# Optimization experiments

Measured on AMD Instinct MI355X. Metric: run time of the kernel, lower is better.

The kernel has to match this reference:

```python
import jax, jax.numpy as jnp
import numpy as np
import math

B, S, H = 2, 2048, 2048
NH, HD, SLOTS = 16, 128, 16


def setup_inputs() -> dict:
    key = jax.random.key(0)
    k1, k2, k3, k4 = jax.random.split(key, 4)
    return {
        "hidden_states": jax.random.normal(k1, (B, S, H), dtype=jnp.float32),
        "stack": jax.random.normal(k2, (B, S, NH, SLOTS, HD), dtype=jnp.float32),
        "mask": jnp.ones((B, S, NH, SLOTS), dtype=jnp.float32),
        "W_action": jax.random.normal(k3, (3 * NH, H), dtype=jnp.float32) * 0.02,
        "b_action": jnp.zeros((3 * NH,), dtype=jnp.float32),
        "W_gate": jax.random.normal(k4, (1, HD), dtype=jnp.float32) * 0.02,
        "b_gate": jnp.zeros((1,), dtype=jnp.float32),
        "res_weight": jnp.ones((1,), dtype=jnp.float32),
    }


def reference(hidden_states, stack, mask, W_action, b_action, W_gate, b_gate, res_weight):
    b, s, h = hidden_states.shape
    nh, slots, hd = stack.shape[2], stack.shape[3], stack.shape[4]

    # action probabilities: push / pop / no-op per head
    logits = (jnp.einsum('bsh,ah->bsa', hidden_states, W_action) + b_action) / math.sqrt(hd)
    actions = jax.nn.softmax(logits.reshape(b, s, nh, 3), axis=-1)  # [B,S,NH,3]

    k_values = hidden_states.reshape(b, s, nh, hd)

    # shifted stack views (slot axis = 3)
    push_stack = jnp.concatenate([k_values[:, :, :, None, :], stack[:, :, :, :-1, :]], axis=3)
    push_mask = jnp.concatenate([jnp.ones_like(mask[:, :, :, :1]), mask[:, :, :, :-1]], axis=3)
    pop_stack = jnp.concatenate([stack[:, :, :, 1:, :], jnp.zeros_like(stack[:, :, :, :1, :])], axis=3)
    pop_mask = jnp.concatenate([mask[:, :, :, 1:], jnp.zeros_like(mask[:, :, :, :1])], axis=3)

    a_push = actions[:, :, :, 0]
    a_pop = actions[:, :, :, 1]
    a_stay = actions[:, :, :, 2]

    new_stack = (a_push[..., None, None] * push_stack
                 + a_pop[..., None, None] * pop_stack
                 + a_stay[..., None, None] * stack)  # [B,S,NH,SLOTS,HD]
    new_mask = (a_push[..., None] * push_mask
                + a_pop[..., None] * pop_mask
                + a_stay[..., None] * mask)  # [B,S,NH,SLOTS]

    # gated readout over slots
    gate_scores = jnp.einsum('bsnkd,d->bsnk', new_stack, W_gate[0]) + b_gate[0]
    gate_weights = jax.nn.softmax(gate_scores + (1.0 - new_mask) * -1e9, axis=-1)
    memory_output = jnp.einsum('bsnkd,bsnk->bsnd', new_stack, gate_weights).reshape(b, s, h)

    output = memory_output * res_weight + hidden_states
    return output, new_stack, new_mask
```

## Files before the change

kernel.cpp:

```cpp
#include <hip/hip_runtime.h>

#define Bc 2
#define Sc 2048
#define Hc 2048
#define NHc 16
#define HDc 128
#define SLOTSc 16
#define NROWS (Bc * Sc)

typedef float v2f __attribute__((ext_vector_type(2)));

__global__ __launch_bounds__(512, 4) void stack_fused(
    const float* __restrict__ hidden,
    const float* __restrict__ stack,
    const float* __restrict__ mask,
    const float* __restrict__ W_action,
    const float* __restrict__ b_action,
    const float* __restrict__ W_gate,
    const float* __restrict__ b_gate,
    const float* __restrict__ res_weight,
    float* __restrict__ out,
    float* __restrict__ new_stack,
    float* __restrict__ new_mask)
{
    __shared__ float hid[Hc];

    const int bs   = blockIdx.x >> 1;
    const int half = blockIdx.x & 1;
    const int tid  = threadIdx.x;
    const int lane = tid & 63;
    const int wave = tid >> 6;
    const int n    = half * 8 + wave;

    const float4* hrow4 = (const float4*)(hidden + (size_t)bs * Hc);
    ((float4*)hid)[tid] = hrow4[tid];
    __syncthreads();

    float s0 = 0.f, s1 = 0.f, s2 = 0.f;
    {
        const float4* hl = (const float4*)hid;
        const float4* W0 = (const float4*)(W_action + (size_t)(3 * n) * Hc);
        const float4* W1 = W0 + (Hc / 4);
        const float4* W2 = W1 + (Hc / 4);
        #pragma unroll 2
        for (int j = 0; j < 8; ++j) {
            float4 a  = hl[lane + j * 64];
            float4 b0 = W0[lane + j * 64];
            float4 b1 = W1[lane + j * 64];
            float4 b2 = W2[lane + j * 64];
            s0 = fmaf(a.x, b0.x, fmaf(a.y, b0.y, fmaf(a.z, b0.z, fmaf(a.w, b0.w, s0))));
            s1 = fmaf(a.x, b1.x, fmaf(a.y, b1.y, fmaf(a.z, b1.z, fmaf(a.w, b1.w, s1))));
            s2 = fmaf(a.x, b2.x, fmaf(a.y, b2.y, fmaf(a.z, b2.z, fmaf(a.w, b2.w, s2))));
        }
    }

    __builtin_amdgcn_sched_barrier(0);
    const size_t sbase = ((size_t)bs * NHc + n) * (size_t)(SLOTSc * HDc);
    const v2f* st2 = (const v2f*)(stack + sbase);
    v2f sv[SLOTSc];
    #pragma unroll
    for (int k = 0; k < SLOTSc; ++k) sv[k] = st2[k * 64 + lane];

    const int cls = lane & 15;
    const int grp = lane & 48;
    float m_d = mask[((size_t)bs * NHc + n) * SLOTSc + cls];
    v2f wg = *(const v2f*)(W_gate + 2 * lane);
    v2f kv = *(const v2f*)(hid + n * HDc + 2 * lane);
    __builtin_amdgcn_sched_barrier(0);

    #pragma unroll
    for (int o = 32; o; o >>= 1) {
        s0 += __shfl_xor(s0, o, 64);
        s1 += __shfl_xor(s1, o, 64);
        s2 += __shfl_xor(s2, o, 64);
    }
    const float scale = 0.08838834764831845f;
    float l0 = (s0 + b_action[3 * n + 0]) * scale;
    float l1 = (s1 + b_action[3 * n + 1]) * scale;
    float l2 = (s2 + b_action[3 * n + 2]) * scale;
    float lm = fmaxf(l0, fmaxf(l1, l2));
    float e0 = __expf(l0 - lm), e1 = __expf(l1 - lm), e2 = __expf(l2 - lm);
    float inv3 = 1.f / (e0 + e1 + e2);
    const float a_push = e0 * inv3;
    const float a_pop  = e1 * inv3;
    const float a_stay = e2 * inv3;

    {
        int ap_prev = (grp | (cls == 0 ? 0 : cls - 1)) << 2;
        int ap_next = (grp | (cls == 15 ? 15 : cls + 1)) << 2;
        float m_prev = __int_as_float(__builtin_amdgcn_ds_bpermute(ap_prev, __float_as_int(m_d)));
        float m_next = __int_as_float(__builtin_amdgcn_ds_bpermute(ap_next, __float_as_int(m_d)));
        m_prev = (cls == 0)  ? 1.f : m_prev;
        m_next = (cls == 15) ? 0.f : m_next;
        m_d = a_push * m_prev + a_pop * m_next + a_stay * m_d;
    }
    if (lane < SLOTSc)
        new_mask[((size_t)bs * NHc + n) * SLOTSc + lane] = m_d;

    const float bg = b_gate[0];
    const float rw = res_weight[0];
    v2f* nst2 = (v2f*)(new_stack + sbase);
    float p[SLOTSc];
    {
        v2f prev = kv;
        #pragma unroll
        for (int k = 0; k < SLOTSc; ++k) {
            v2f cur = sv[k];
            v2f nxt;
            if (k < SLOTSc - 1) nxt = sv[k + 1];
            else { nxt.x = 0.f; nxt.y = 0.f; }
            v2f ns;
            ns.x = a_push * prev.x + a_pop * nxt.x + a_stay * cur.x;
            ns.y = a_push * prev.y + a_pop * nxt.y + a_stay * cur.y;
            sv[k] = ns;
            nst2[k * 64 + lane] = ns;
            p[k] = ns.x * wg.x + ns.y * wg.y;
            prev = cur;
        }
    }

    float w8[8];
    #pragma unroll
    for (int j = 0; j < 8; ++j) {
        float a = p[2 * j], b = p[2 * j + 1];
        bool hi = (lane & 1);
        float keep = hi ? b : a;
        float send = hi ? a : b;
        w8[j] = keep + __shfl_xor(send, 1, 64);
    }
    float w4[4];
    #pragma unroll
    for (int j = 0; j < 4; ++j) {
        float a = w8[2 * j], b = w8[2 * j + 1];
        bool hi = (lane & 2);
        float keep = hi ? b : a;
        float send = hi ? a : b;
        w4[j] = keep + __shfl_xor(send, 2, 64);
    }
    float w2[2];
    #pragma unroll
    for (int j = 0; j < 2; ++j) {
        float a = w4[2 * j], b = w4[2 * j + 1];
        bool hi = (lane & 4);
        float keep = hi ? b : a;
        float send = hi ? a : b;
        w2[j] = keep + __shfl_xor(send, 4, 64);
    }
    float u;
    {
        float a = w2[0], b = w2[1];
        bool hi = (lane & 8);
        float keep = hi ? b : a;
        float send = hi ? a : b;
        u = keep + __shfl_xor(send, 8, 64);
    }
    u += __shfl_xor(u, 16, 64);
    u += __shfl_xor(u, 32, 64);

    float g = u + bg + (1.f - m_d) * -1000000000.0f;
    float mx = g;
    mx = fmaxf(mx, __shfl_xor(mx, 1, 64));
    mx = fmaxf(mx, __shfl_xor(mx, 2, 64));
    mx = fmaxf(mx, __shfl_xor(mx, 4, 64));
    mx = fmaxf(mx, __shfl_xor(mx, 8, 64));
    float e = __expf(g - mx);
    float ssum = e;
    ssum += __shfl_xor(ssum, 1, 64);
    ssum += __shfl_xor(ssum, 2, 64);
    ssum += __shfl_xor(ssum, 4, 64);
    ssum += __shfl_xor(ssum, 8, 64);
    float gw_d = e / ssum;

    v2f mo; mo.x = 0.f; mo.y = 0.f;
    const int grpb = grp << 2;
    #pragma unroll
    for (int k = 0; k < SLOTSc; ++k) {
        float gwk = __int_as_float(
            __builtin_amdgcn_ds_bpermute(grpb | (k << 2), __float_as_int(gw_d)));
        mo.x = fmaf(gwk, sv[k].x, mo.x);
        mo.y = fmaf(gwk, sv[k].y, mo.y);
    }
    v2f ov;
    ov.x = mo.x * rw + kv.x;
    ov.y = mo.y * rw + kv.y;
    *(v2f*)(out + (size_t)bs * Hc + n * HDc + 2 * lane) = ov;
}

extern "C" void kernel_launch(void* const* d_in, const int* in_sizes, int n_in,
                              void* d_out, int out_size, void* d_ws, size_t ws_size,
                              hipStream_t stream) {
    const float* hidden     = (const float*)d_in[0];
    const float* stack      = (const float*)d_in[1];
    const float* mask       = (const float*)d_in[2];
    const float* W_action   = (const float*)d_in[3];
    const float* b_action   = (const float*)d_in[4];
    const float* W_gate     = (const float*)d_in[5];
    const float* b_gate     = (const float*)d_in[6];
    const float* res_weight = (const float*)d_in[7];

    float* out       = (float*)d_out;
    float* new_stack = out + (size_t)Bc * Sc * Hc;
    float* new_mask  = new_stack + (size_t)Bc * Sc * NHc * SLOTSc * HDc;

    hipLaunchKernelGGL(stack_fused, dim3(NROWS * 2), dim3(512), 0, stream,
                       hidden, stack, mask, W_action, b_action,
                       W_gate, b_gate, res_weight,
                       out, new_stack, new_mask);
}
```

Before: 239.3 us.

## Process four rows per block to reuse action weights across rows

New measurement: 240.0 us. No clear change (+0.3%).

```diff
diff --git a/kernel.cpp b/kernel.cpp
--- a/kernel.cpp
+++ b/kernel.cpp
@@ -7,6 +7,7 @@
 #define HDc 128
 #define SLOTSc 16
 #define NROWS (Bc * Sc)
+#define RPB 4
 
 typedef float v2f __attribute__((ext_vector_type(2)));
 
@@ -23,167 +24,200 @@
     float* __restrict__ new_stack,
     float* __restrict__ new_mask)
 {
-    __shared__ float hid[Hc];
-
-    const int bs   = blockIdx.x >> 1;
+    __shared__ float hid[RPB * Hc];
+
+    const int bs0  = (blockIdx.x >> 1) * RPB;
     const int half = blockIdx.x & 1;
     const int tid  = threadIdx.x;
     const int lane = tid & 63;
     const int wave = tid >> 6;
     const int n    = half * 8 + wave;
 
-    const float4* hrow4 = (const float4*)(hidden + (size_t)bs * Hc);
-    ((float4*)hid)[tid] = hrow4[tid];
+    {
+        const float4* hrow4 = (const float4*)(hidden + (size_t)bs0 * Hc);
+        float4* hl4 = (float4*)hid;
+        #pragma unroll
+        for (int r = 0; r < RPB; ++r)
+            hl4[r * 512 + tid] = hrow4[r * 512 + tid];
+    }
     __syncthreads();
 
-    float s0 = 0.f, s1 = 0.f, s2 = 0.f;
+    float s0[RPB], s1[RPB], s2[RPB];
+    #pragma unroll
+    for (int r = 0; r < RPB; ++r) { s0[r] = 0.f; s1[r] = 0.f; s2[r] = 0.f; }
     {
-        const float4* hl = (const float4*)hid;
         const float4* W0 = (const float4*)(W_action + (size_t)(3 * n) * Hc);
         const float4* W1 = W0 + (Hc / 4);
         const float4* W2 = W1 + (Hc / 4);
-        #pragma unroll 2
-        for (int j = 0; j < 8; ++j) {
-            float4 a  = hl[lane + j * 64];
-            float4 b0 = W0[lane + j * 64];
-            float4 b1 = W1[lane + j * 64];
-            float4 b2 = W2[lane + j * 64];
-            s0 = fmaf(a.x, b0.x, fmaf(a.y, b0.y, fmaf(a.z, b0.z, fmaf(a.w, b0.w, s0))));
-            s1 = fmaf(a.x, b1.x, fmaf(a.y, b1.y, fmaf(a.z, b1.z, fmaf(a.w, b1.w, s1))));
-            s2 = fmaf(a.x, b2.x, fmaf(a.y, b2.y, fmaf(a.z, b2.z, fmaf(a.w, b2.w, s2))));
-        }
-    }
-
-    __builtin_amdgcn_sched_barrier(0);
-    const size_t sbase = ((size_t)bs * NHc + n) * (size_t)(SLOTSc * HDc);
-    const v2f* st2 = (const v2f*)(stack + sbase);
-    v2f sv[SLOTSc];
+        const float4* hl4 = (const float4*)hid;
+        #pragma unroll
+        for (int h = 0; h < 2; ++h) {
+            float4 w0[4], w1[4], w2[4];
+            #pragma unroll
+            for (int j = 0; j < 4; ++j) {
+                w0[j] = W0[h * 256 + j * 64 + lane];
+                w1[j] = W1[h * 256 + j * 64 + lane];
+                w2[j] = W2[h * 256 + j * 64 + lane];
+            }
+            #pragma unroll
+            for (int r = 0; r < RPB; ++r) {
+                #pragma unroll
+                for (int j = 0; j < 4; ++j) {
+                    float4 a = hl4[r * 512 + h * 256 + j * 64 + lane];
+                    s0[r] = fmaf(a.x, w0[j].x, fmaf(a.y, w0[j].y, fmaf(a.z, w0[j].z, fmaf(a.w, w0[j].w, s0[r]))));
+                    s1[r] = fmaf(a.x, w1[j].x, fmaf(a.y, w1[j].y, fmaf(a.z, w1[j].z, fmaf(a.w, w1[j].w, s1[r]))));
+                    s2[r] = fmaf(a.x, w2[j].x, fmaf(a.y, w2[j].y, fmaf(a.z, w2[j].z, fmaf(a.w, w2[j].w, s2[r]))));
+                }
+            }
+        }
+    }
+
+    const float ba0 = b_action[3 * n + 0];
+    const float ba1 = b_action[3 * n + 1];
+    const float ba2 = b_action[3 * n + 2];
+
+    float apu[RPB], apo[RPB], ast[RPB];
     #pragma unroll
-    for (int k = 0; k < SLOTSc; ++k) sv[k] = st2[k * 64 + lane];
+    for (int r = 0; r < RPB; ++r) {
+        float t0 = s0[r], t1 = s1[r], t2 = s2[r];
+        #pragma unroll
+        for (int o = 32; o; o >>= 1) {
+            t0 += __shfl_xor(t0, o, 64);
+            t1 += __shfl_xor(t1, o, 64);
+            t2 += __shfl_xor(t2, o, 64);
+        }
+        const float scale = 0.08838834764831845f;
+        float l0 = (t0 + ba0) * scale;
+        float l1 = (t1 + ba1) * scale;
+        float l2 = (t2 + ba2) * scale;
+        float lm = fmaxf(l0, fmaxf(l1, l2));
+        float e0 = __expf(l0 - lm), e1 = __expf(l1 - lm), e2 = __expf(l2 - lm);
+        float inv3 = 1.f / (e0 + e1 + e2);
+        apu[r] = e0 * inv3;
+        apo[r] = e1 * inv3;
+        ast[r] = e2 * inv3;
+    }
 
     const int cls = lane & 15;
     const int grp = lane & 48;
-    float m_d = mask[((size_t)bs * NHc + n) * SLOTSc + cls];
     v2f wg = *(const v2f*)(W_gate + 2 * lane);
-    v2f kv = *(const v2f*)(hid + n * HDc + 2 * lane);
-    __builtin_amdgcn_sched_barrier(0);
-
-    #pragma unroll
-    for (int o = 32; o; o >>= 1) {
-        s0 += __shfl_xor(s0, o, 64);
-        s1 += __shfl_xor(s1, o, 64);
-        s2 += __shfl_xor(s2, o, 64);
-    }
-    const float scale = 0.08838834764831845f;
-    float l0 = (s0 + b_action[3 * n + 0]) * scale;
-    float l1 = (s1 + b_action[3 * n + 1]) * scale;
-    float l2 = (s2 + b_action[3 * n + 2]) * scale;
-    float lm = fmaxf(l0, fmaxf(l1, l2));
-    float e0 = __expf(l0 - lm), e1 = __expf(l1 - lm), e2 = __expf(l2 - lm);
-    float inv3 = 1.f / (e0 + e1 + e2);
-    const float a_push = e0 * inv3;
-    const float a_pop  = e1 * inv3;
-    const float a_stay = e2 * inv3;
-
-    {
-        int ap_prev = (grp | (cls == 0 ? 0 : cls - 1)) << 2;
-        int ap_next = (grp | (cls == 15 ? 15 : cls + 1)) << 2;
-        float m_prev = __int_as_float(__builtin_amdgcn_ds_bpermute(ap_prev, __float_as_int(m_d)));
-        float m_next = __int_as_float(__builtin_amdgcn_ds_bpermute(ap_next, __float_as_int(m_d)));
-        m_prev = (cls == 0)  ? 1.f : m_prev;
-        m_next = (cls == 15) ? 0.f : m_next;
-        m_d = a_push * m_prev + a_pop * m_next + a_stay * m_d;
-    }
-    if (lane < SLOTSc)
-        new_mask[((size_t)bs * NHc + n) * SLOTSc + lane] = m_d;
-
     const float bg = b_gate[0];
     const float rw = res_weight[0];
-    v2f* nst2 = (v2f*)(new_stack + sbase);
-    float p[SLOTSc];
-    {
-        v2f prev = kv;
+
+    #pragma unroll
+    for (int r = 0; r < RPB; ++r) {
+        const int bs = bs0 + r;
+        const float a_push = apu[r];
+        const float a_pop  = apo[r];
+        const float a_stay = ast[r];
+
+        const size_t sbase = ((size_t)bs * NHc + n) * (size_t)(SLOTSc * HDc);
+        const v2f* st2 = (const v2f*)(stack + sbase);
+        v2f sv[SLOTSc];
+        #pragma unroll
+        for (int k = 0; k < SLOTSc; ++k) sv[k] = st2[k * 64 + lane];
+
+        v2f kv = *(const v2f*)(hid + r * Hc + n * HDc + 2 * lane);
+        float m_d = mask[((size_t)bs * NHc + n) * SLOTSc + cls];
+
+        {
+            int ap_prev = (grp | (cls == 0 ? 0 : cls - 1)) << 2;
+            int ap_next = (grp | (cls == 15 ? 15 : cls + 1)) << 2;
+            float m_prev = __int_as_float(__builtin_amdgcn_ds_bpermute(ap_prev, __float_as_int(m_d)));
+            float m_next = __int_as_float(__builtin_amdgcn_ds_bpermute(ap_next, __float_as_int(m_d)));
+            m_prev = (cls == 0)  ? 1.f : m_prev;
+            m_next = (cls == 15) ? 0.f : m_next;
+            m_d = a_push * m_prev + a_pop * m_next + a_stay * m_d;
+        }
+        if (lane < SLOTSc)
+            new_mask[((size_t)bs * NHc + n) * SLOTSc + lane] = m_d;
+
+        v2f* nst2 = (v2f*)(new_stack + sbase);
+        float p[SLOTSc];
+        {
+            v2f prev = kv;
+            #pragma unroll
+            for (int k = 0; k < SLOTSc; ++k) {
+                v2f cur = sv[k];
+                v2f nxt;
+                if (k < SLOTSc - 1) nxt = sv[k + 1];
+                else { nxt.x = 0.f; nxt.y = 0.f; }
+                v2f ns;
+                ns.x = a_push * prev.x + a_pop * nxt.x + a_stay * cur.x;
+                ns.y = a_push * prev.y + a_pop * nxt.y + a_stay * cur.y;
+                sv[k] = ns;
+                nst2[k * 64 + lane] = ns;
+                p[k] = ns.x * wg.x + ns.y * wg.y;
+                prev = cur;
+            }
+        }
+
+        float w8[8];
+        #pragma unroll
+        for (int j = 0; j < 8; ++j) {
+            float a = p[2 * j], b = p[2 * j + 1];
+            bool hi = (lane & 1);
+            float keep = hi ? b : a;
+            float send = hi ? a : b;
+            w8[j] = keep + __shfl_xor(send, 1, 64);
+        }
+        float w4[4];
+        #pragma unroll
+        for (int j = 0; j < 4; ++j) {
+            float a = w8[2 * j], b = w8[2 * j + 1];
+            bool hi = (lane & 2);
+            float keep = hi ? b : a;
+            float send = hi ? a : b;
+            w4[j] = keep + __shfl_xor(send, 2, 64);
+        }
+        float w2[2];
+        #pragma unroll
+        for (int j = 0; j < 2; ++j) {
+            float a = w4[2 * j], b = w4[2 * j + 1];
+            bool hi = (lane & 4);
+            float keep = hi ? b : a;
+            float send = hi ? a : b;
+            w2[j] = keep + __shfl_xor(send, 4, 64);
+        }
+        float u;
+        {
+            float a = w2[0], b = w2[1];
+            bool hi = (lane & 8);
+            float keep = hi ? b : a;
+            float send = hi ? a : b;
+            u = keep + __shfl_xor(send, 8, 64);
+        }
+        u += __shfl_xor(u, 16, 64);
+        u += __shfl_xor(u, 32, 64);
+
+        float g = u + bg + (1.f - m_d) * -1000000000.0f;
+        float mx = g;
+        mx = fmaxf(mx, __shfl_xor(mx, 1, 64));
+        mx = fmaxf(mx, __shfl_xor(mx, 2, 64));
+        mx = fmaxf(mx, __shfl_xor(mx, 4, 64));
+        mx = fmaxf(mx, __shfl_xor(mx, 8, 64));
+        float e = __expf(g - mx);
+        float ssum = e;
+        ssum += __shfl_xor(ssum, 1, 64);
+        ssum += __shfl_xor(ssum, 2, 64);
+        ssum += __shfl_xor(ssum, 4, 64);
+        ssum += __shfl_xor(ssum, 8, 64);
+        float gw_d = e / ssum;
+
+        v2f mo; mo.x = 0.f; mo.y = 0.f;
+        const int grpb = grp << 2;
         #pragma unroll
         for (int k = 0; k < SLOTSc; ++k) {
-            v2f cur = sv[k];
-            v2f nxt;
-            if (k < SLOTSc - 1) nxt = sv[k + 1];
-            else { nxt.x = 0.f; nxt.y = 0.f; }
-            v2f ns;
-            ns.x = a_push * prev.x + a_pop * nxt.x + a_stay * cur.x;
-            ns.y = a_push * prev.y + a_pop * nxt.y + a_stay * cur.y;
-            sv[k] = ns;
-            nst2[k * 64 + lane] = ns;
-            p[k] = ns.x * wg.x + ns.y * wg.y;
-            prev = cur;
-        }
-    }
-
-    float w8[8];
-    #pragma unroll
-    for (int j = 0; j < 8; ++j) {
-        float a = p[2 * j], b = p[2 * j + 1];
-        bool hi = (lane & 1);
-        float keep = hi ? b : a;
-        float send = hi ? a : b;
-        w8[j] = keep + __shfl_xor(send, 1, 64);
-    }
-    float w4[4];
-    #pragma unroll
-    for (int j = 0; j < 4; ++j) {
-        float a = w8[2 * j], b = w8[2 * j + 1];
-        bool hi = (lane & 2);
-        float keep = hi ? b : a;
-        float send = hi ? a : b;
-        w4[j] = keep + __shfl_xor(send, 2, 64);
-    }
-    float w2[2];
-    #pragma unroll
-    for (int j = 0; j < 2; ++j) {
-        float a = w4[2 * j], b = w4[2 * j + 1];
-        bool hi = (lane & 4);
-        float keep = hi ? b : a;
-        float send = hi ? a : b;
-        w2[j] = keep + __shfl_xor(send, 4, 64);
-    }
-    float u;
-    {
-        float a = w2[0], b = w2[1];
-        bool hi = (lane & 8);
-        float keep = hi ? b : a;
-        float send = hi ? a : b;
-        u = keep + __shfl_xor(send, 8, 64);
-    }
-    u += __shfl_xor(u, 16, 64);
-    u += __shfl_xor(u, 32, 64);
-
-    float g = u + bg + (1.f - m_d) * -1000000000.0f;
-    float mx = g;
-    mx = fmaxf(mx, __shfl_xor(mx, 1, 64));
-    mx = fmaxf(mx, __shfl_xor(mx, 2, 64));
-    mx = fmaxf(mx, __shfl_xor(mx, 4, 64));
-    mx = fmaxf(mx, __shfl_xor(mx, 8, 64));
-    float e = __expf(g - mx);
-    float ssum = e;
-    ssum += __shfl_xor(ssum, 1, 64);
-    ssum += __shfl_xor(ssum, 2, 64);
-    ssum += __shfl_xor(ssum, 4, 64);
-    ssum += __shfl_xor(ssum, 8, 64);
-    float gw_d = e / ssum;
-
-    v2f mo; mo.x = 0.f; mo.y = 0.f;
-    const int grpb = grp << 2;
-    #pragma unroll
-    for (int k = 0; k < SLOTSc; ++k) {
-        float gwk = __int_as_float(
-            __builtin_amdgcn_ds_bpermute(grpb | (k << 2), __float_as_int(gw_d)));
-        mo.x = fmaf(gwk, sv[k].x, mo.x);
-        mo.y = fmaf(gwk, sv[k].y, mo.y);
-    }
-    v2f ov;
-    ov.x = mo.x * rw + kv.x;
-    ov.y = mo.y * rw + kv.y;
-    *(v2f*)(out + (size_t)bs * Hc + n * HDc + 2 * lane) = ov;
+            float gwk = __int_as_float(
+                __builtin_amdgcn_ds_bpermute(grpb | (k << 2), __float_as_int(gw_d)));
+            mo.x = fmaf(gwk, sv[k].x, mo.x);
+            mo.y = fmaf(gwk, sv[k].y, mo.y);
+        }
+        v2f ov;
+        ov.x = mo.x * rw + kv.x;
+        ov.y = mo.y * rw + kv.y;
+        *(v2f*)(out + (size_t)bs * Hc + n * HDc + 2 * lane) = ov;
+    }
 }
 
 extern "C" void kernel_launch(void* const* d_in, const int* in_sizes, int n_in,
@@ -202,7 +236,7 @@
     float* new_stack = out + (size_t)Bc * Sc * Hc;
     float* new_mask  = new_stack + (size_t)Bc * Sc * NHc * SLOTSc * HDc;
 
-    hipLaunchKernelGGL(stack_fused, dim3(NROWS * 2), dim3(512), 0, stream,
+    hipLaunchKernelGGL(stack_fused, dim3((NROWS / RPB) * 2), dim3(512), 0, stream,
                        hidden, stack, mask, W_action, b_action,
                        W_gate, b_gate, res_weight,
                        out, new_stack, new_mask);
```

## Convert fused stack kernel to persistent grid with register double-buffered prefetch

Applied to the files above, without the earlier changes.

Result: slower. 565.9 us (+136.5%).

```diff
diff --git a/kernel.cpp b/kernel.cpp
--- a/kernel.cpp
+++ b/kernel.cpp
@@ -7,84 +7,18 @@
 #define HDc 128
 #define SLOTSc 16
 #define NROWS (Bc * Sc)
+#define NU (NROWS * 4)
+#define GRIDB 768
 
 typedef float v2f __attribute__((ext_vector_type(2)));
 
-__global__ __launch_bounds__(512, 4) void stack_fused(
-    const float* __restrict__ hidden,
-    const float* __restrict__ stack,
-    const float* __restrict__ mask,
-    const float* __restrict__ W_action,
-    const float* __restrict__ b_action,
-    const float* __restrict__ W_gate,
-    const float* __restrict__ b_gate,
-    const float* __restrict__ res_weight,
-    float* __restrict__ out,
-    float* __restrict__ new_stack,
+__device__ __forceinline__ void unit_chain(
+    v2f (&sv)[SLOTSc], const float a_push, const float a_pop, const float a_stay,
+    float m_d, const v2f kv, const v2f wg, const float bg, const float rw,
+    const int row, const int n, const int lane, const int cls, const int grp,
+    float* __restrict__ out, float* __restrict__ new_stack,
     float* __restrict__ new_mask)
 {
-    __shared__ float hid[Hc];
-
-    const int bs   = blockIdx.x >> 1;
-    const int half = blockIdx.x & 1;
-    const int tid  = threadIdx.x;
-    const int lane = tid & 63;
-    const int wave = tid >> 6;
-    const int n    = half * 8 + wave;
-
-    const float4* hrow4 = (const float4*)(hidden + (size_t)bs * Hc);
-    ((float4*)hid)[tid] = hrow4[tid];
-    __syncthreads();
-
-    float s0 = 0.f, s1 = 0.f, s2 = 0.f;
-    {
-        const float4* hl = (const float4*)hid;
-        const float4* W0 = (const float4*)(W_action + (size_t)(3 * n) * Hc);
-        const float4* W1 = W0 + (Hc / 4);
-        const float4* W2 = W1 + (Hc / 4);
-        #pragma unroll 2
-        for (int j = 0; j < 8; ++j) {
-            float4 a  = hl[lane + j * 64];
-            float4 b0 = W0[lane + j * 64];
-            float4 b1 = W1[lane + j * 64];
-            float4 b2 = W2[lane + j * 64];
-            s0 = fmaf(a.x, b0.x, fmaf(a.y, b0.y, fmaf(a.z, b0.z, fmaf(a.w, b0.w, s0))));
-            s1 = fmaf(a.x, b1.x, fmaf(a.y, b1.y, fmaf(a.z, b1.z, fmaf(a.w, b1.w, s1))));
-            s2 = fmaf(a.x, b2.x, fmaf(a.y, b2.y, fmaf(a.z, b2.z, fmaf(a.w, b2.w, s2))));
-        }
-    }
-
-    __builtin_amdgcn_sched_barrier(0);
-    const size_t sbase = ((size_t)bs * NHc + n) * (size_t)(SLOTSc * HDc);
-    const v2f* st2 = (const v2f*)(stack + sbase);
-    v2f sv[SLOTSc];
-    #pragma unroll
-    for (int k = 0; k < SLOTSc; ++k) sv[k] = st2[k * 64 + lane];
-
-    const int cls = lane & 15;
-    const int grp = lane & 48;
-    float m_d = mask[((size_t)bs * NHc + n) * SLOTSc + cls];
-    v2f wg = *(const v2f*)(W_gate + 2 * lane);
-    v2f kv = *(const v2f*)(hid + n * HDc + 2 * lane);
-    __builtin_amdgcn_sched_barrier(0);
-
-    #pragma unroll
-    for (int o = 32; o; o >>= 1) {
-        s0 += __shfl_xor(s0, o, 64);
-        s1 += __shfl_xor(s1, o, 64);
-        s2 += __shfl_xor(s2, o, 64);
-    }
-    const float scale = 0.08838834764831845f;
-    float l0 = (s0 + b_action[3 * n + 0]) * scale;
-    float l1 = (s1 + b_action[3 * n + 1]) * scale;
-    float l2 = (s2 + b_action[3 * n + 2]) * scale;
-    float lm = fmaxf(l0, fmaxf(l1, l2));
-    float e0 = __expf(l0 - lm), e1 = __expf(l1 - lm), e2 = __expf(l2 - lm);
-    float inv3 = 1.f / (e0 + e1 + e2);
-    const float a_push = e0 * inv3;
-    const float a_pop  = e1 * inv3;
-    const float a_stay = e2 * inv3;
-
     {
         int ap_prev = (grp | (cls == 0 ? 0 : cls - 1)) << 2;
         int ap_next = (grp | (cls == 15 ? 15 : cls + 1)) << 2;
@@ -95,10 +29,9 @@
         m_d = a_push * m_prev + a_pop * m_next + a_stay * m_d;
     }
     if (lane < SLOTSc)
-        new_mask[((size_t)bs * NHc + n) * SLOTSc + lane] = m_d;
-
-    const float bg = b_gate[0];
-    const float rw = res_weight[0];
+        new_mask[((size_t)row * NHc + n) * SLOTSc + lane] = m_d;
+
+    const size_t sbase = ((size_t)row * NHc + n) * (size_t)(SLOTSc * HDc);
     v2f* nst2 = (v2f*)(new_stack + sbase);
     float p[SLOTSc];
     {
@@ -183,7 +116,137 @@
     v2f ov;
     ov.x = mo.x * rw + kv.x;
     ov.y = mo.y * rw + kv.y;
-    *(v2f*)(out + (size_t)bs * Hc + n * HDc + 2 * lane) = ov;
+    *(v2f*)(out + (size_t)row * Hc + n * HDc + 2 * lane) = ov;
+}
+
+__global__ __launch_bounds__(256, 3) void stack_persist(
+    const float* __restrict__ hidden,
+    const float* __restrict__ stack,
+    const float* __restrict__ mask,
+    const float* __restrict__ W_action,
+    const float* __restrict__ b_action,
+    const float* __restrict__ W_gate,
+    const float* __restrict__ b_gate,
+    const float* __restrict__ res_weight,
+    float* __restrict__ out,
+    float* __restrict__ new_stack,
+    float* __restrict__ new_mask)
+{
+    __shared__ float hid[2][Hc];
+
+    const int tid  = threadIdx.x;
+    const int lane = tid & 63;
+    const int wave = tid >> 6;
+    const int q    = blockIdx.x & 3;
+    const int n    = q * 4 + wave;
+    const int cls  = lane & 15;
+    const int grp  = lane & 48;
+
+    v2f wg = *(const v2f*)(W_gate + 2 * lane);
+    const float bg  = b_gate[0];
+    const float rw  = res_weight[0];
+    const float ba0 = b_action[3 * n + 0];
+    const float ba1 = b_action[3 * n + 1];
+    const float ba2 = b_action[3 * n + 2];
+    const float4* W0 = (const float4*)(W_action + (size_t)(3 * n) * Hc);
+    const float4* W1 = W0 + (Hc / 4);
+    const float4* W2 = W1 + (Hc / 4);
+
+    v2f svA[SLOTSc], svB[SLOTSc];
+    float m_cur, m_nxt;
+
+    int u = blockIdx.x;
+    {
+        const int row = u >> 2;
+        const float4* hr = (const float4*)(hidden + (size_t)row * Hc);
+        float4 h0 = hr[tid];
+        float4 h1 = hr[256 + tid];
+        const size_t sb = ((size_t)row * NHc + n) * (size_t)(SLOTSc * HDc);
+        const v2f* st2 = (const v2f*)(stack + sb);
+        #pragma unroll
+        for (int k = 0; k < SLOTSc; ++k) svA[k] = st2[k * 64 + lane];
+        m_cur = mask[((size_t)row * NHc + n) * SLOTSc + cls];
+        ((float4*)hid[0])[tid] = h0;
+        ((float4*)hid[0])[256 + tid] = h1;
+    }
+    __syncthreads();
+
+    int cur = 0;
+    bool phase = true;
+    const float scale = 0.08838834764831845f;
+
+    while (true) {
+        const int row  = u >> 2;
+        const int un   = u + GRIDB;
+        const bool pref = (un < NU);
+
+        float s0 = 0.f, s1 = 0.f, s2 = 0.f;
+        {
+            const float4* hl4 = (const float4*)hid[cur];
+            #pragma unroll 2
+            for (int j = 0; j < 8; ++j) {
+                float4 a  = hl4[lane + j * 64];
+                float4 b0 = W0[lane + j * 64];
+                float4 b1 = W1[lane + j * 64];
+                float4 b2 = W2[lane + j * 64];
+                s0 = fmaf(a.x, b0.x, fmaf(a.y, b0.y, fmaf(a.z, b0.z, fmaf(a.w, b0.w, s0))));
+                s1 = fmaf(a.x, b1.x, fmaf(a.y, b1.y, fmaf(a.z, b1.z, fmaf(a.w, b1.w, s1))));
+                s2 = fmaf(a.x, b2.x, fmaf(a.y, b2.y, fmaf(a.z, b2.z, fmaf(a.w, b2.w, s2))));
+            }
+        }
+        #pragma unroll
+        for (int o = 32; o; o >>= 1) {
+            s0 += __shfl_xor(s0, o, 64);
+            s1 += __shfl_xor(s1, o, 64);
+            s2 += __shfl_xor(s2, o, 64);
+        }
+        float l0 = (s0 + ba0) * scale;
+        float l1 = (s1 + ba1) * scale;
+        float l2 = (s2 + ba2) * scale;
+        float lm = fmaxf(l0, fmaxf(l1, l2));
+        float e0 = __expf(l0 - lm), e1 = __expf(l1 - lm), e2 = __expf(l2 - lm);
+        float inv3 = 1.f / (e0 + e1 + e2);
+        const float a_push = e0 * inv3;
+        const float a_pop  = e1 * inv3;
+        const float a_stay = e2 * inv3;
+
+        v2f kv = *(const v2f*)(&hid[cur][n * HDc + 2 * lane]);
+
+        float4 h0n, h1n;
+        if (pref) {
+            const int rown = un >> 2;
+            const float4* hr = (const float4*)(hidden + (size_t)rown * Hc);
+            h0n = hr[tid];
+            h1n = hr[256 + tid];
+            const size_t sbn = ((size_t)rown * NHc + n) * (size_t)(SLOTSc * HDc);
+            const v2f* stn = (const v2f*)(stack + sbn);
+            if (phase) {
+                #pragma unroll
+                for (int k = 0; k < SLOTSc; ++k) svB[k] = stn[k * 64 + lane];
+            } else {
+                #pragma unroll
+                for (int k = 0; k < SLOTSc; ++k) svA[k] = stn[k * 64 + lane];
+            }
+            m_nxt = mask[((size_t)rown * NHc + n) * SLOTSc + cls];
+        }
+
+        if (phase)
+            unit_chain(svA, a_push, a_pop, a_stay, m_cur, kv, wg, bg, rw,
+                       row, n, lane, cls, grp, out, new_stack, new_mask);
+        else
+            unit_chain(svB, a_push, a_pop, a_stay, m_cur, kv, wg, bg, rw,
+                       row, n, lane, cls, grp, out, new_stack, new_mask);
+
+        if (!pref) break;
+
+        ((float4*)hid[cur ^ 1])[tid] = h0n;
+        ((float4*)hid[cur ^ 1])[256 + tid] = h1n;
+        __syncthreads();
+        cur ^= 1;
+        phase = !phase;
+        m_cur = m_nxt;
+        u = un;
+    }
 }
 
 extern "C" void kernel_launch(void* const* d_in, const int* in_sizes, int n_in,
@@ -202,7 +265,7 @@
     float* new_stack = out + (size_t)Bc * Sc * Hc;
     float* new_mask  = new_stack + (size_t)Bc * Sc * NHc * SLOTSc * HDc;
 
-    hipLaunchKernelGGL(stack_fused, dim3(NROWS * 2), dim3(512), 0, stream,
+    hipLaunchKernelGGL(stack_persist, dim3(GRIDB), dim3(256), 0, stream,
                        hidden, stack, mask, W_action, b_action,
                        W_gate, b_gate, res_weight,
                        out, new_stack, new_mask);
```

## Process both head halves per block and prefetch second stack tile early

Applied to the files above, without the earlier changes.

Result: slower. 253.6 us (+6.0%).

```diff
diff --git a/kernel.cpp b/kernel.cpp
--- a/kernel.cpp
+++ b/kernel.cpp
@@ -10,7 +10,7 @@
 
 typedef float v2f __attribute__((ext_vector_type(2)));
 
-__global__ __launch_bounds__(512, 4) void stack_fused(
+__global__ __launch_bounds__(512, 4) void stack_fused2(
     const float* __restrict__ hidden,
     const float* __restrict__ stack,
     const float* __restrict__ mask,
@@ -25,26 +25,40 @@
 {
     __shared__ float hid[Hc];
 
-    const int bs   = blockIdx.x >> 1;
-    const int half = blockIdx.x & 1;
+    const int row  = blockIdx.x;
     const int tid  = threadIdx.x;
     const int lane = tid & 63;
     const int wave = tid >> 6;
-    const int n    = half * 8 + wave;
-
-    const float4* hrow4 = (const float4*)(hidden + (size_t)bs * Hc);
-    ((float4*)hid)[tid] = hrow4[tid];
+    const int n0   = wave;
+    const int n1   = 8 + wave;
+    const int cls  = lane & 15;
+    const int grp  = lane & 48;
+    const float scale = 0.08838834764831845f;
+
+    ((float4*)hid)[tid] = ((const float4*)(hidden + (size_t)row * Hc))[tid];
+
+    const size_t sbase0 = ((size_t)row * NHc + n0) * (size_t)(SLOTSc * HDc);
+    const v2f* stA = (const v2f*)(stack + sbase0);
+    v2f svA[SLOTSc];
+    #pragma unroll
+    for (int k = 0; k < SLOTSc; ++k) svA[k] = stA[k * 64 + lane];
+    float m0 = mask[((size_t)row * NHc + n0) * SLOTSc + cls];
+
+    v2f wg = *(const v2f*)(W_gate + 2 * lane);
+    const float bg = b_gate[0];
+    const float rw = res_weight[0];
+
     __syncthreads();
 
     float s0 = 0.f, s1 = 0.f, s2 = 0.f;
     {
-        const float4* hl = (const float4*)hid;
-        const float4* W0 = (const float4*)(W_action + (size_t)(3 * n) * Hc);
+        const float4* hl4 = (const float4*)hid;
+        const float4* W0 = (const float4*)(W_action + (size_t)(3 * n0) * Hc);
         const float4* W1 = W0 + (Hc / 4);
         const float4* W2 = W1 + (Hc / 4);
         #pragma unroll 2
         for (int j = 0; j < 8; ++j) {
-            float4 a  = hl[lane + j * 64];
+            float4 a  = hl4[lane + j * 64];
             float4 b0 = W0[lane + j * 64];
             float4 b1 = W1[lane + j * 64];
             float4 b2 = W2[lane + j * 64];
@@ -54,19 +68,12 @@
         }
     }
 
-    __builtin_amdgcn_sched_barrier(0);
-    const size_t sbase = ((size_t)bs * NHc + n) * (size_t)(SLOTSc * HDc);
-    const v2f* st2 = (const v2f*)(stack + sbase);
-    v2f sv[SLOTSc];
+    const size_t sbase1 = ((size_t)row * NHc + n1) * (size_t)(SLOTSc * HDc);
+    const v2f* stB = (const v2f*)(stack + sbase1);
+    v2f svB[SLOTSc];
     #pragma unroll
-    for (int k = 0; k < SLOTSc; ++k) sv[k] = st2[k * 64 + lane];
-
-    const int cls = lane & 15;
-    const int grp = lane & 48;
-    float m_d = mask[((size_t)bs * NHc + n) * SLOTSc + cls];
-    v2f wg = *(const v2f*)(W_gate + 2 * lane);
-    v2f kv = *(const v2f*)(hid + n * HDc + 2 * lane);
-    __builtin_amdgcn_sched_barrier(0);
+    for (int k = 0; k < SLOTSc; ++k) svB[k] = stB[k * 64 + lane];
+    float m1 = mask[((size_t)row * NHc + n1) * SLOTSc + cls];
 
     #pragma unroll
     for (int o = 32; o; o >>= 1) {
@@ -74,116 +81,248 @@
         s1 += __shfl_xor(s1, o, 64);
         s2 += __shfl_xor(s2, o, 64);
     }
-    const float scale = 0.08838834764831845f;
-    float l0 = (s0 + b_action[3 * n + 0]) * scale;
-    float l1 = (s1 + b_action[3 * n + 1]) * scale;
-    float l2 = (s2 + b_action[3 * n + 2]) * scale;
+    float l0 = (s0 + b_action[3 * n0 + 0]) * scale;
+    float l1 = (s1 + b_action[3 * n0 + 1]) * scale;
+    float l2 = (s2 + b_action[3 * n0 + 2]) * scale;
     float lm = fmaxf(l0, fmaxf(l1, l2));
     float e0 = __expf(l0 - lm), e1 = __expf(l1 - lm), e2 = __expf(l2 - lm);
     float inv3 = 1.f / (e0 + e1 + e2);
-    const float a_push = e0 * inv3;
-    const float a_pop  = e1 * inv3;
-    const float a_stay = e2 * inv3;
+    float a_push = e0 * inv3;
+    float a_pop  = e1 * inv3;
+    float a_stay = e2 * inv3;
 
     {
-        int ap_prev = (grp | (cls == 0 ? 0 : cls - 1)) << 2;
-        int ap_next = (grp | (cls == 15 ? 15 : cls + 1)) << 2;
-        float m_prev = __int_as_float(__builtin_amdgcn_ds_bpermute(ap_prev, __float_as_int(m_d)));
-        float m_next = __int_as_float(__builtin_amdgcn_ds_bpermute(ap_next, __float_as_int(m_d)));
-        m_prev = (cls == 0)  ? 1.f : m_prev;
-        m_next = (cls == 15) ? 0.f : m_next;
-        m_d = a_push * m_prev + a_pop * m_next + a_stay * m_d;
-    }
-    if (lane < SLOTSc)
-        new_mask[((size_t)bs * NHc + n) * SLOTSc + lane] = m_d;
-
-    const float bg = b_gate[0];
-    const float rw = res_weight[0];
-    v2f* nst2 = (v2f*)(new_stack + sbase);
-    float p[SLOTSc];
+        {
+            int ap_prev = (grp | (cls == 0 ? 0 : cls - 1)) << 2;
+            int ap_next = (grp | (cls == 15 ? 15 : cls + 1)) << 2;
+            float m_prev = __int_as_float(__builtin_amdgcn_ds_bpermute(ap_prev, __float_as_int(m0)));
+            float m_next = __int_as_float(__builtin_amdgcn_ds_bpermute(ap_next, __float_as_int(m0)));
+            m_prev = (cls == 0)  ? 1.f : m_prev;
+            m_next = (cls == 15) ? 0.f : m_next;
+            m0 = a_push * m_prev + a_pop * m_next + a_stay * m0;
+        }
+        if (lane < SLOTSc)
+            new_mask[((size_t)row * NHc + n0) * SLOTSc + lane] = m0;
+
+        v2f kv = *(const v2f*)(hid + n0 * HDc + 2 * lane);
+        v2f* nst2 = (v2f*)(new_stack + sbase0);
+
+        float w8[8];
+        {
+            v2f prev = kv;
+            float pe = 0.f;
+            #pragma unroll
+            for (int k = 0; k < SLOTSc; ++k) {
+                v2f cur = svA[k];
+                v2f nxt;
+                if (k < SLOTSc - 1) nxt = svA[k + 1];
+                else { nxt.x = 0.f; nxt.y = 0.f; }
+                v2f ns;
+                ns.x = a_push * prev.x + a_pop * nxt.x + a_stay * cur.x;
+                ns.y = a_push * prev.y + a_pop * nxt.y + a_stay * cur.y;
+                svA[k] = ns;
+                nst2[k * 64 + lane] = ns;
+                float pk = ns.x * wg.x + ns.y * wg.y;
+                if ((k & 1) == 0) pe = pk;
+                else {
+                    bool hi = (lane & 1);
+                    float keep = hi ? pk : pe;
+                    float send = hi ? pe : pk;
+                    w8[k >> 1] = keep + __shfl_xor(send, 1, 64);
+                }
+                prev = cur;
+            }
+        }
+        float w4[4];
+        #pragma unroll
+        for (int j = 0; j < 4; ++j) {
+            float a = w8[2 * j], b = w8[2 * j + 1];
+            bool hi = (lane & 2);
+            float keep = hi ? b : a;
+            float send = hi ? a : b;
+            w4[j] = keep + __shfl_xor(send, 2, 64);
+        }
+        float w2[2];
+        #pragma unroll
+        for (int j = 0; j < 2; ++j) {
+            float a = w4[2 * j], b = w4[2 * j + 1];
+            bool hi = (lane & 4);
+            float keep = hi ? b : a;
+            float send = hi ? a : b;
+            w2[j] = keep + __shfl_xor(send, 4, 64);
+        }
+        float u;
+        {
+            float a = w2[0], b = w2[1];
+            bool hi = (lane & 8);
+            float keep = hi ? b : a;
+            float send = hi ? a : b;
+            u = keep + __shfl_xor(send, 8, 64);
+        }
+        u += __shfl_xor(u, 16, 64);
+        u += __shfl_xor(u, 32, 64);
+
+        float g = u + bg + (1.f - m0) * -1000000000.0f;
+        float mx = g;
+        mx = fmaxf(mx, __shfl_xor(mx, 1, 64));
+        mx = fmaxf(mx, __shfl_xor(mx, 2, 64));
+        mx = fmaxf(mx, __shfl_xor(mx, 4, 64));
+        mx = fmaxf(mx, __shfl_xor(mx, 8, 64));
+        float e = __expf(g - mx);
+        float ssum = e;
+        ssum += __shfl_xor(ssum, 1, 64);
+        ssum += __shfl_xor(ssum, 2, 64);
+        ssum += __shfl_xor(ssum, 4, 64);
+        ssum += __shfl_xor(ssum, 8, 64);
+        float gw_d = e / ssum;
+
+        v2f mo; mo.x = 0.f; mo.y = 0.f;
+        const int grpb = grp << 2;
+        #pragma unroll
+        for (int k = 0; k < SLOTSc; ++k) {
+            float gwk = __int_as_float(
+                __builtin_amdgcn_ds_bpermute(grpb | (k << 2), __float_as_int(gw_d)));
+            mo.x = fmaf(gwk, svA[k].x, mo.x);
+            mo.y = fmaf(gwk, svA[k].y, mo.y);
+        }
+        v2f ov;
+        ov.x = mo.x * rw + kv.x;
+        ov.y = mo.y * rw + kv.y;
+        *(v2f*)(out + (size_t)row * Hc + n0 * HDc + 2 * lane) = ov;
+    }
+
+    s0 = 0.f; s1 = 0.f; s2 = 0.f;
     {
-        v2f prev = kv;
+        const float4* hl4 = (const float4*)hid;
+        const float4* W0 = (const float4*)(W_action + (size_t)(3 * n1) * Hc);
+        const float4* W1 = W0 + (Hc / 4);
+        const float4* W2 = W1 + (Hc / 4);
+        #pragma unroll 2
+        for (int j = 0; j < 8; ++j) {
+            float4 a  = hl4[lane + j * 64];
+            float4 b0 = W0[lane + j * 64];
+            float4 b1 = W1[lane + j * 64];
+            float4 b2 = W2[lane + j * 64];
+            s0 = fmaf(a.x, b0.x, fmaf(a.y, b0.y, fmaf(a.z, b0.z, fmaf(a.w, b0.w, s0))));
+            s1 = fmaf(a.x, b1.x, fmaf(a.y, b1.y, fmaf(a.z, b1.z, fmaf(a.w, b1.w, s1))));
+            s2 = fmaf(a.x, b2.x, fmaf(a.y, b2.y, fmaf(a.z, b2.z, fmaf(a.w, b2.w, s2))));
+        }
+    }
+    #pragma unroll
+    for (int o = 32; o; o >>= 1) {
+        s0 += __shfl_xor(s0, o, 64);
+        s1 += __shfl_xor(s1, o, 64);
+        s2 += __shfl_xor(s2, o, 64);
+    }
+    l0 = (s0 + b_action[3 * n1 + 0]) * scale;
+    l1 = (s1 + b_action[3 * n1 + 1]) * scale;
+    l2 = (s2 + b_action[3 * n1 + 2]) * scale;
+    lm = fmaxf(l0, fmaxf(l1, l2));
+    e0 = __expf(l0 - lm); e1 = __expf(l1 - lm); e2 = __expf(l2 - lm);
+    inv3 = 1.f / (e0 + e1 + e2);
+    a_push = e0 * inv3;
+    a_pop  = e1 * inv3;
+    a_stay = e2 * inv3;
+
+    {
+        {
+            int ap_prev = (grp | (cls == 0 ? 0 : cls - 1)) << 2;
+            int ap_next = (grp | (cls == 15 ? 15 : cls + 1)) << 2;
+            float m_prev = __int_as_float(__builtin_amdgcn_ds_bpermute(ap_prev, __float_as_int(m1)));
+            float m_next = __int_as_float(__builtin_amdgcn_ds_bpermute(ap_next, __float_as_int(m1)));
+            m_prev = (cls == 0)  ? 1.f : m_prev;
+            m_next = (cls == 15) ? 0.f : m_next;
+            m1 = a_push * m_prev + a_pop * m_next + a_stay * m1;
+        }
+        if (lane < SLOTSc)
+            new_mask[((size_t)row * NHc + n1) * SLOTSc + lane] = m1;
+
+        v2f kv = *(const v2f*)(hid + n1 * HDc + 2 * lane);
+        v2f* nst2 = (v2f*)(new_stack + sbase1);
+
+        float w8[8];
+        {
+            v2f prev = kv;
+            float pe = 0.f;
+            #pragma unroll
+            for (int k = 0; k < SLOTSc; ++k) {
+                v2f cur = svB[k];
+                v2f nxt;
+                if (k < SLOTSc - 1) nxt = svB[k + 1];
+                else { nxt.x = 0.f; nxt.y = 0.f; }
+                v2f ns;
+                ns.x = a_push * prev.x + a_pop * nxt.x + a_stay * cur.x;
+                ns.y = a_push * prev.y + a_pop * nxt.y + a_stay * cur.y;
+                svB[k] = ns;
+                nst2[k * 64 + lane] = ns;
+                float pk = ns.x * wg.x + ns.y * wg.y;
+                if ((k & 1) == 0) pe = pk;
+                else {
+                    bool hi = (lane & 1);
+                    float keep = hi ? pk : pe;
+                    float send = hi ? pe : pk;
+                    w8[k >> 1] = keep + __shfl_xor(send, 1, 64);
+                }
+                prev = cur;
+            }
+        }
+        float w4[4];
+        #pragma unroll
+        for (int j = 0; j < 4; ++j) {
+            float a = w8[2 * j], b = w8[2 * j + 1];
+            bool hi = (lane & 2);
+            float keep = hi ? b : a;
+            float send = hi ? a : b;
+            w4[j] = keep + __shfl_xor(send, 2, 64);
+        }
+        float w2[2];
+        #pragma unroll
+        for (int j = 0; j < 2; ++j) {
+            float a = w4[2 * j], b = w4[2 * j + 1];
+            bool hi = (lane & 4);
+            float keep = hi ? b : a;
+            float send = hi ? a : b;
+            w2[j] = keep + __shfl_xor(send, 4, 64);
+        }
+        float u;
+        {
+            float a = w2[0], b = w2[1];
+            bool hi = (lane & 8);
+            float keep = hi ? b : a;
+            float send = hi ? a : b;
+            u = keep + __shfl_xor(send, 8, 64);
+        }
+        u += __shfl_xor(u, 16, 64);
+        u += __shfl_xor(u, 32, 64);
+
+        float g = u + bg + (1.f - m1) * -1000000000.0f;
+        float mx = g;
+        mx = fmaxf(mx, __shfl_xor(mx, 1, 64));
+        mx = fmaxf(mx, __shfl_xor(mx, 2, 64));
+        mx = fmaxf(mx, __shfl_xor(mx, 4, 64));
+        mx = fmaxf(mx, __shfl_xor(mx, 8, 64));
+        float e = __expf(g - mx);
+        float ssum = e;
+        ssum += __shfl_xor(ssum, 1, 64);
+        ssum += __shfl_xor(ssum, 2, 64);
+        ssum += __shfl_xor(ssum, 4, 64);
+        ssum += __shfl_xor(ssum, 8, 64);
+        float gw_d = e / ssum;
+
+        v2f mo; mo.x = 0.f; mo.y = 0.f;
+        const int grpb = grp << 2;
         #pragma unroll
         for (int k = 0; k < SLOTSc; ++k) {
-            v2f cur = sv[k];
-            v2f nxt;
-            if (k < SLOTSc - 1) nxt = sv[k + 1];
-            else { nxt.x = 0.f; nxt.y = 0.f; }
-            v2f ns;
-            ns.x = a_push * prev.x + a_pop * nxt.x + a_stay * cur.x;
-            ns.y = a_push * prev.y + a_pop * nxt.y + a_stay * cur.y;
-            sv[k] = ns;
-            nst2[k * 64 + lane] = ns;
-            p[k] = ns.x * wg.x + ns.y * wg.y;
-            prev = cur;
-        }
-    }
-
-    float w8[8];
-    #pragma unroll
-    for (int j = 0; j < 8; ++j) {
-        float a = p[2 * j], b = p[2 * j + 1];
-        bool hi = (lane & 1);
-        float keep = hi ? b : a;
-        float send = hi ? a : b;
-        w8[j] = keep + __shfl_xor(send, 1, 64);
-    }
-    float w4[4];
-    #pragma unroll
-    for (int j = 0; j < 4; ++j) {
-        float a = w8[2 * j], b = w8[2 * j + 1];
-        bool hi = (lane & 2);
-        float keep = hi ? b : a;
-        float send = hi ? a : b;
-        w4[j] = keep + __shfl_xor(send, 2, 64);
-    }
-    float w2[2];
-    #pragma unroll
-    for (int j = 0; j < 2; ++j) {
-        float a = w4[2 * j], b = w4[2 * j + 1];
-        bool hi = (lane & 4);
-        float keep = hi ? b : a;
-        float send = hi ? a : b;
-        w2[j] = keep + __shfl_xor(send, 4, 64);
-    }
-    float u;
-    {
-        float a = w2[0], b = w2[1];
-        bool hi = (lane & 8);
-        float keep = hi ? b : a;
-        float send = hi ? a : b;
-        u = keep + __shfl_xor(send, 8, 64);
-    }
-    u += __shfl_xor(u, 16, 64);
-    u += __shfl_xor(u, 32, 64);
-
-    float g = u + bg + (1.f - m_d) * -1000000000.0f;
-    float mx = g;
-    mx = fmaxf(mx, __shfl_xor(mx, 1, 64));
-    mx = fmaxf(mx, __shfl_xor(mx, 2, 64));
-    mx = fmaxf(mx, __shfl_xor(mx, 4, 64));
-    mx = fmaxf(mx, __shfl_xor(mx, 8, 64));
-    float e = __expf(g - mx);
-    float ssum = e;
-    ssum += __shfl_xor(ssum, 1, 64);
-    ssum += __shfl_xor(ssum, 2, 64);
-    ssum += __shfl_xor(ssum, 4, 64);
-    ssum += __shfl_xor(ssum, 8, 64);
-    float gw_d = e / ssum;
-
-    v2f mo; mo.x = 0.f; mo.y = 0.f;
-    const int grpb = grp << 2;
-    #pragma unroll
-    for (int k = 0; k < SLOTSc; ++k) {
-        float gwk = __int_as_float(
-            __builtin_amdgcn_ds_bpermute(grpb | (k << 2), __float_as_int(gw_d)));
-        mo.x = fmaf(gwk, sv[k].x, mo.x);
-        mo.y = fmaf(gwk, sv[k].y, mo.y);
-    }
-    v2f ov;
-    ov.x = mo.x * rw + kv.x;
-    ov.y = mo.y * rw + kv.y;
-    *(v2f*)(out + (size_t)bs * Hc + n * HDc + 2 * lane) = ov;
+            float gwk = __int_as_float(
+                __builtin_amdgcn_ds_bpermute(grpb | (k << 2), __float_as_int(gw_d)));
+            mo.x = fmaf(gwk, svB[k].x, mo.x);
+            mo.y = fmaf(gwk, svB[k].y, mo.y);
+        }
+        v2f ov;
+        ov.x = mo.x * rw + kv.x;
+        ov.y = mo.y * rw + kv.y;
+        *(v2f*)(out + (size_t)row * Hc + n1 * HDc + 2 * lane) = ov;
+    }
 }
 
 extern "C" void kernel_launch(void* const* d_in, const int* in_sizes, int n_in,
@@ -202,7 +341,7 @@
     float* new_stack = out + (size_t)Bc * Sc * Hc;
     float* new_mask  = new_stack + (size_t)Bc * Sc * NHc * SLOTSc * HDc;
 
-    hipLaunchKernelGGL(stack_fused, dim3(NROWS * 2), dim3(512), 0, stream,
+    hipLaunchKernelGGL(stack_fused2, dim3(NROWS), dim3(512), 0, stream,
                        hidden, stack, mask, W_action, b_action,
                        W_gate, b_gate, res_weight,
                        out, new_stack, new_mask);
```
